# Kernel optimization log

Measured on AMD Instinct MI355X. Metric: run time of the kernel, lower is better.

Reference implementation:

```python
import jax, jax.numpy as jnp
import numpy as np

TEMPERATURE = 0.1


def setup_inputs() -> dict:
    key = jax.random.key(0)
    k1, k2 = jax.random.split(key)
    N, D = 8192, 128
    features = jax.random.normal(k1, (N, D), dtype=jnp.float32)
    labels = jax.random.randint(k2, (N,), 0, 1000, dtype=jnp.int64)
    return {"features": features, "labels": labels}


def reference(features, labels):
    N = features.shape[0]
    # L2-normalize rows
    feats = features / jnp.linalg.norm(features, axis=1, keepdims=True)
    # positive-pair mask from labels [N, N]
    labels = labels.reshape(-1, 1)
    mask = (labels == labels.T).astype(feats.dtype)
    # similarity matrix scaled by temperature
    sim = jnp.matmul(feats, feats.T) / TEMPERATURE
    # exclude self-comparisons (diagonal)
    logits_mask = 1.0 - jnp.eye(N, dtype=feats.dtype)
    mask = mask * logits_mask
    exp_logits = jnp.exp(sim) * logits_mask
    log_prob = sim - jnp.log(exp_logits.sum(axis=1, keepdims=True) + 1e-9)
    mask_sum = mask.sum(axis=1)
    mask_sum = jnp.where(mask_sum == 0, jnp.ones_like(mask_sum), mask_sum)
    mean_log_prob_pos = (mask * log_prob).sum(axis=1) / mask_sum
    return -mean_log_prob_pos.mean()
```

## Files before the change

### kernel.cpp

```cpp
#include <hip/hip_runtime.h>
#include <hip/hip_bf16.h>
#include <math.h>


constexpr int N = 8192;
constexpr int D = 128;

typedef __attribute__((ext_vector_type(8))) short short8;
typedef __attribute__((ext_vector_type(4))) float f32x4;

constexpr float SELF_POISON = -50.0f;

__device__ __forceinline__ float fast_exp2(float x) {
#if __has_builtin(__builtin_amdgcn_exp2f)
    return __builtin_amdgcn_exp2f(x);
#else
    return __expf(x * 0.69314718056f);
#endif
}

__global__ void prep_kernel(const float* __restrict__ F,
                            unsigned int* __restrict__ FbP,
                            float* __restrict__ out) {
    if (blockIdx.x == 0 && threadIdx.x == 0) out[0] = 0.0f;
    int row = blockIdx.x * 4 + (threadIdx.x >> 6);
    int l = threadIdx.x & 63;
    float2 v = ((const float2*)(F + (size_t)row * D))[l];
    float ss = v.x * v.x + v.y * v.y;
#pragma unroll
    for (int off = 32; off > 0; off >>= 1) ss += __shfl_xor(ss, off);
    float sc = sqrtf(14.4269504089f / ss);
    __hip_bfloat16 hx = __float2bfloat16(v.x * sc);
    __hip_bfloat16 hy = __float2bfloat16(v.y * sc);
    unsigned int ux = *(unsigned short*)&hx;
    unsigned int uy = *(unsigned short*)&hy;
    unsigned int idx = ((unsigned)(row >> 4) << 10) | ((unsigned)(l >> 2) << 6) |
                       ((unsigned)(row & 15) << 2) | (unsigned)(l & 3);
    FbP[idx] = ux | (uy << 16);
}

#define LOADB(BUF, TJ, KK)                                          \
    _Pragma("unroll") for (int n_ = 0; n_ < 4; ++n_)                \
        BUF[n_] = P[((TJ) * 8 + wx * 4 + n_) * 256 + (KK) * 64 + l];

#define MFMASTEP(BUF, KK)                                           \
    _Pragma("unroll") for (int m_ = 0; m_ < 4; ++m_)                \
        _Pragma("unroll") for (int n_ = 0; n_ < 4; ++n_)            \
            acc[m_][n_] = __builtin_amdgcn_mfma_f32_16x16x32_bf16(  \
                Af[KK][m_], BUF[n_], acc[m_][n_], 0, 0, 0);

__global__ __launch_bounds__(256, 2) void sim_kernel(
    const short8* __restrict__ P, const int* __restrict__ labels,
    float* __restrict__ partE, float* __restrict__ partP) {
    const int g2 = blockIdx.x & 7;
    const int ti = blockIdx.x >> 3;
    const int tjs = g2 * 8;
    const int i0 = ti * 128;

    const int t = threadIdx.x, w = t >> 6, l = t & 63;
    const int c = l & 15, quad = l >> 4;
    const int wy = w >> 1, wx = w & 1;

    short8 Af[4][4];
#pragma unroll
    for (int kk = 0; kk < 4; ++kk)
#pragma unroll
        for (int m = 0; m < 4; ++m)
            Af[kk][m] = P[(ti * 8 + wy * 4 + m) * 256 + kk * 64 + l];

    int li[4][4];
#pragma unroll
    for (int m = 0; m < 4; ++m)
#pragma unroll
        for (int r = 0; r < 4; ++r)
            li[m][r] = labels[i0 + wy * 64 + m * 16 + quad * 4 + r];

    const bool selfQuad = (quad == (c >> 2));

    float RE[4][4] = {}, RP[4][4] = {};

    short8 bfA[4], bfB[4];
    LOADB(bfA, tjs, 0);
    LOADB(bfB, tjs, 1);

#pragma unroll 1
    for (int tj = tjs; tj < tjs + 8; ++tj) {
        const int j0 = tj * 128;
        int lj[4];
#pragma unroll
        for (int n = 0; n < 4; ++n) lj[n] = labels[j0 + wx * 64 + n * 16 + c];

        f32x4 acc[4][4] = {};
        const int tp = (tj < tjs + 7) ? tj + 1 : tjs;
        MFMASTEP(bfA, 0);
        LOADB(bfA, tj, 2);
        MFMASTEP(bfB, 1);
        LOADB(bfB, tj, 3);
        MFMASTEP(bfA, 2);
        LOADB(bfA, tp, 0);
        MFMASTEP(bfB, 3);
        LOADB(bfB, tp, 1);

        if (tj == ti && wy == wx) {
#pragma unroll
            for (int m = 0; m < 4; ++m)
#pragma unroll
                for (int r = 0; r < 4; ++r) {
                    bool cond = selfQuad && (r == (c & 3));
                    acc[m][m][r] = cond ? SELF_POISON : acc[m][m][r];
                }
        }

#pragma unroll
        for (int m = 0; m < 4; ++m) {
#pragma unroll
            for (int n = 0; n < 4; ++n) {
#pragma unroll
                for (int r = 0; r < 4; ++r) {
                    float s2 = acc[m][n][r];
                    RE[m][r] += fast_exp2(s2);
                    RP[m][r] += (li[m][r] == lj[n]) ? s2 : 0.0f;
                }
            }
        }
    }

#pragma unroll
    for (int m = 0; m < 4; ++m)
#pragma unroll
        for (int r = 0; r < 4; ++r) {
#pragma unroll
            for (int off = 1; off < 16; off <<= 1) {
                RE[m][r] += __shfl_xor(RE[m][r], off);
                RP[m][r] += __shfl_xor(RP[m][r], off);
            }
        }
    if (c == 0) {
        if ((ti >> 3) == g2 && wy == wx) {
#pragma unroll
            for (int m = 0; m < 4; ++m)
#pragma unroll
                for (int r = 0; r < 4; ++r) RP[m][r] -= SELF_POISON;
        }
        const int slot = g2 * 2 + wx;
#pragma unroll
        for (int m = 0; m < 4; ++m)
#pragma unroll
            for (int r = 0; r < 4; ++r) {
                int gi = i0 + wy * 64 + m * 16 + quad * 4 + r;
                partE[(size_t)gi * 16 + slot] = RE[m][r];
                partP[(size_t)gi * 16 + slot] = RP[m][r];
            }
    }
}

__global__ void reduce_kernel(const float* __restrict__ partE,
                              const float* __restrict__ partP,
                              const int* __restrict__ labels,
                              float* __restrict__ out) {
    __shared__ int hist[1024];
    __shared__ float ws4[4];
    const int t = threadIdx.x, w = t >> 6, l = t & 63;
    const int half = l >> 5, sl = l & 31;
    const int rbase = blockIdx.x * 64 + w * 16;

#pragma unroll
    for (int k = 0; k < 4; ++k) hist[t + 256 * k] = 0;
    __syncthreads();
#pragma unroll
    for (int k = 0; k < 32; ++k) atomicAdd(&hist[labels[t + 256 * k]], 1);
    __syncthreads();

    float a = 0.0f;
#pragma unroll
    for (int it = 0; it < 8; ++it) {
        int row = rbase + it * 2 + half;
        float se = 0.0f, sp = 0.0f;
        if (sl < 16) {
            se = partE[(size_t)row * 16 + sl];
            sp = partP[(size_t)row * 16 + sl];
        }
#pragma unroll
        for (int off = 1; off < 32; off <<= 1) {
            se += __shfl_xor(se, off);
            sp += __shfl_xor(sp, off);
        }
        if (sl == 0) {
            int cnt = hist[labels[row]] - 1;
            if (cnt > 0)
                a += logf(se + 1e-9f) - 0.69314718056f * sp / (float)cnt;
        }
    }
#pragma unroll
    for (int off = 1; off < 64; off <<= 1) a += __shfl_xor(a, off);
    if (l == 0) ws4[w] = a;
    __syncthreads();
    if (t == 0) {
        float s = ws4[0] + ws4[1] + ws4[2] + ws4[3];
        atomicAdd(out, s * (1.0f / (float)N));
    }
}

extern "C" void kernel_launch(void* const* d_in, const int* in_sizes, int n_in,
                              void* d_out, int out_size, void* d_ws, size_t ws_size,
                              hipStream_t stream) {
    const float* F      = (const float*)d_in[0];
    const int*   labels = (const int*)d_in[1];
    float* out = (float*)d_out;

    unsigned int* FbP = (unsigned int*)d_ws;
    float* partE = (float*)((char*)d_ws + (size_t)2 * 1024 * 1024);
    float* partP = partE + (size_t)N * 16;

    prep_kernel<<<N / 4, 256, 0, stream>>>(F, FbP, out);
    sim_kernel<<<512, 256, 0, stream>>>((const short8*)FbP, labels, partE,
                                        partP);
    reduce_kernel<<<128, 256, 0, stream>>>(partE, partP, labels, out);
}
```

Baseline: 93.81 us.

## Fuse final reduction into sim kernel via last-block-per-row-tile counter

Removes the separate reduce kernel launch. Each of the 8 blocks covering a 128-row tile bumps a global atomic counter, and the last one to finish reduces the partial exp-sums and positive-sums for those rows and atomically adds into the output. This saves a kernel launch and its gap, but the last block for each tile rebuilds a 1024-bin label histogram over all 8192 labels, and it adds threadfence/atomic synchronisation plus LDS use in the main kernel.

```diff
diff --git a/kernel.cpp b/kernel.cpp
--- a/kernel.cpp
+++ b/kernel.cpp
@@ -21,8 +21,12 @@
 
 __global__ void prep_kernel(const float* __restrict__ F,
                             unsigned int* __restrict__ FbP,
-                            float* __restrict__ out) {
-    if (blockIdx.x == 0 && threadIdx.x == 0) out[0] = 0.0f;
+                            float* __restrict__ out,
+                            int* __restrict__ cnt) {
+    if (blockIdx.x == 0) {
+        if (threadIdx.x == 0) out[0] = 0.0f;
+        if (threadIdx.x < 64) cnt[threadIdx.x] = 0;
+    }
     int row = blockIdx.x * 4 + (threadIdx.x >> 6);
     int l = threadIdx.x & 63;
     float2 v = ((const float2*)(F + (size_t)row * D))[l];
@@ -51,7 +55,12 @@
 
 __global__ __launch_bounds__(256, 2) void sim_kernel(
     const short8* __restrict__ P, const int* __restrict__ labels,
-    float* __restrict__ partE, float* __restrict__ partP) {
+    float* __restrict__ partE, float* __restrict__ partP,
+    int* __restrict__ cnt, float* __restrict__ out) {
+    __shared__ int hist[1024];
+    __shared__ float ws4[4];
+    __shared__ int isLast;
+
     const int g2 = blockIdx.x & 7;
     const int ti = blockIdx.x >> 3;
     const int tjs = g2 * 8;
@@ -152,17 +161,15 @@
                 partP[(size_t)gi * 16 + slot] = RP[m][r];
             }
     }
-}
-
-__global__ void reduce_kernel(const float* __restrict__ partE,
-                              const float* __restrict__ partP,
-                              const int* __restrict__ labels,
-                              float* __restrict__ out) {
-    __shared__ int hist[1024];
-    __shared__ float ws4[4];
-    const int t = threadIdx.x, w = t >> 6, l = t & 63;
-    const int half = l >> 5, sl = l & 31;
-    const int rbase = blockIdx.x * 64 + w * 16;
+
+    __syncthreads();
+    if (t == 0) {
+        __threadfence();
+        isLast = (atomicAdd(&cnt[ti], 1) == 7);
+    }
+    __syncthreads();
+    if (!isLast) return;
+    __threadfence();
 
 #pragma unroll
     for (int k = 0; k < 4; ++k) hist[t + 256 * k] = 0;
@@ -171,10 +178,11 @@
     for (int k = 0; k < 32; ++k) atomicAdd(&hist[labels[t + 256 * k]], 1);
     __syncthreads();
 
+    const int hw = t >> 5, sl = l & 31;
     float a = 0.0f;
-#pragma unroll
-    for (int it = 0; it < 8; ++it) {
-        int row = rbase + it * 2 + half;
+#pragma unroll 1
+    for (int it = 0; it < 16; ++it) {
+        int row = i0 + it * 8 + hw;
         float se = 0.0f, sp = 0.0f;
         if (sl < 16) {
             se = partE[(size_t)row * 16 + sl];
@@ -186,9 +194,9 @@
             sp += __shfl_xor(sp, off);
         }
         if (sl == 0) {
-            int cnt = hist[labels[row]] - 1;
-            if (cnt > 0)
-                a += logf(se + 1e-9f) - 0.69314718056f * sp / (float)cnt;
+            int cn = hist[labels[row]] - 1;
+            if (cn > 0)
+                a += logf(se + 1e-9f) - 0.69314718056f * sp / (float)cn;
         }
     }
 #pragma unroll
@@ -211,9 +219,9 @@
     unsigned int* FbP = (unsigned int*)d_ws;
     float* partE = (float*)((char*)d_ws + (size_t)2 * 1024 * 1024);
     float* partP = partE + (size_t)N * 16;
-
-    prep_kernel<<<N / 4, 256, 0, stream>>>(F, FbP, out);
+    int*   cnt   = (int*)(partP + (size_t)N * 16);
+
+    prep_kernel<<<N / 4, 256, 0, stream>>>(F, FbP, out, cnt);
     sim_kernel<<<512, 256, 0, stream>>>((const short8*)FbP, labels, partE,
-                                        partP);
-    reduce_kernel<<<128, 256, 0, stream>>>(partE, partP, labels, out);
-}
+                                        partP, cnt, out);
+}
```

After: 123.9 us. 1.32x slower.
